# Optimization experiments

Hardware: AMD Instinct MI355X
Metric: run time of the kernel (lower is better)

The kernel has to match this reference:

```python
import jax, jax.numpy as jnp
import numpy as np

HEADS = 8
D_MODEL = 512

def setup_inputs() -> dict:
    key = jax.random.key(0)
    ks = jax.random.split(key, 7)
    t, w, h, b = 8, 14, 14, 8
    seq = t * w * h + 1  # 1569, includes CLS token
    q = jax.random.normal(ks[0], (seq, b, D_MODEL), jnp.float32)
    k = jax.random.normal(ks[1], (seq, b, D_MODEL), jnp.float32)
    value = jax.random.normal(ks[2], (seq, b, D_MODEL), jnp.float32)
    in_proj_weight = jax.random.normal(ks[3], (3 * D_MODEL, D_MODEL), jnp.float32) * (D_MODEL ** -0.5)
    in_proj_bias = jax.random.normal(ks[4], (3 * D_MODEL,), jnp.float32) * 0.02
    out_w = jax.random.normal(ks[5], (D_MODEL, D_MODEL), jnp.float32) * (D_MODEL ** -0.5)
    out_b = jax.random.normal(ks[6], (D_MODEL,), jnp.float32) * 0.02
    return {"q": q, "k": k, "value": value,
            "in_proj_weight": in_proj_weight, "in_proj_bias": in_proj_bias,
            "out_w": out_w, "out_b": out_b, "t": t, "w": w, "h": h}

def _sdpa(q, k, v):
    # scaled dot-product attention over batched 3D tensors [B, L, dh]
    temp = q.shape[-1] ** 0.5
    scores = jnp.einsum('bqd,bkd->bqk', q, k) / temp
    a = jax.nn.softmax(scores, axis=-1)  # softmax over dim=2 == last dim
    return jnp.einsum('bqk,bkd->bqd', a, v), a

def reference(q, k, value, in_proj_weight, in_proj_bias, out_w, out_b, t, w, h):
    seq, b, c = q.shape
    H, dh, wh = HEADS, c // HEADS, w * h
    q_cls = q[:1]          # [1, b, c] passed through untouched
    x = q[1:]              # [t*wh, b, c]
    qkv = x @ in_proj_weight.T + in_proj_bias  # fused QKV proj
    qq, kk, vv = qkv[..., :c], qkv[..., c:2 * c], qkv[..., 2 * c:]
    to5 = lambda z: z.reshape(t, wh, b, H, dh)
    # spatial stage: batch = (H, b, t), attend over wh
    q_s = to5(qq).transpose(3, 2, 0, 1, 4).reshape(H * b * t, wh, dh)
    k_s = to5(kk).transpose(3, 2, 0, 1, 4).reshape(H * b * t, wh, dh)
    v_s = to5(vv).transpose(3, 2, 0, 1, 4).reshape(H * b * t, wh, dh)
    out_s, attn = _sdpa(q_s, k_s, v_s)
    # temporal stage: batch = (H, b, wh), attend over t; V comes from spatial output
    v_t = out_s.reshape(H, b, t, wh, dh).transpose(0, 1, 3, 2, 4).reshape(H * b * wh, t, dh)
    q_t = to5(qq).transpose(3, 2, 1, 0, 4).reshape(H * b * wh, t, dh)
    k_t = to5(kk).transpose(3, 2, 1, 0, 4).reshape(H * b * wh, t, dh)
    out_t, _ = _sdpa(q_t, k_t, v_t)
    # back to [t*wh, b, c]
    out = out_t.reshape(H, b, wh, t, dh).transpose(3, 2, 1, 0, 4).reshape(t * wh, b, c)
    out = out @ out_w.T + out_b
    return jnp.concatenate([q_cls, out], axis=0), attn
```

## Files before the change

kernel.cpp:

```cpp
#include <hip/hip_runtime.h>
#include <cstdint>
#include <cstddef>

typedef __bf16 bf16;
typedef __bf16 bf16x8 __attribute__((ext_vector_type(8)));
typedef __bf16 bf16x4 __attribute__((ext_vector_type(4)));
typedef float  f32x4  __attribute__((ext_vector_type(4)));

#define MFMA16(a, b, c) __builtin_amdgcn_mfma_f32_16x16x32_bf16(a, b, c, 0, 0, 0)

__device__ __forceinline__ void gl2lds16(const bf16* g, bf16* l) {
  __builtin_amdgcn_global_load_lds(
      (const __attribute__((address_space(1))) void*)g,
      (__attribute__((address_space(3))) void*)l, 16, 0, 0);
}

__device__ __forceinline__ void cvt4(const float* __restrict__ s, bf16* __restrict__ d) {
  f32x4 v = *(const f32x4*)s;
  bf16x4 o;
  o[0] = (bf16)v[0]; o[1] = (bf16)v[1]; o[2] = (bf16)v[2]; o[3] = (bf16)v[3];
  *(bf16x4*)d = o;
}

__global__ __launch_bounds__(256) void prep_kernel(
    const float* __restrict__ q, const float* __restrict__ win,
    const float* __restrict__ wout, float* __restrict__ out0,
    bf16* __restrict__ xb, bf16* __restrict__ wqb, bf16* __restrict__ wob) {
  long u = (long)blockIdx.x * 256 + threadIdx.x;
  const long NX4 = 1605632, NWQ4 = 196608, NWO4 = 65536, NQC4 = 1024;
  if (u < NX4) { cvt4(q + 4096 + u * 4, xb + u * 4); return; }
  u -= NX4;
  if (u < NWQ4) { cvt4(win + u * 4, wqb + u * 4); return; }
  u -= NWQ4;
  if (u < NWO4) { cvt4(wout + u * 4, wob + u * 4); return; }
  u -= NWO4;
  if (u < NQC4) { *(f32x4*)(out0 + u * 4) = *(const f32x4*)(q + u * 4); }
}

template <bool OUTF32>
__global__ __launch_bounds__(256) void gemm_bt(
    const bf16* __restrict__ A, const bf16* __restrict__ Bm,
    const float* __restrict__ bias, bf16* __restrict__ Cb,
    float* __restrict__ Cf, int N, int K, long coff) {
  __shared__ bf16 As[128 * 32];
  __shared__ bf16 Bs[128 * 32];
  const int tid = threadIdx.x;
  const int wid = tid >> 6, lane = tid & 63;
  const int lr = lane & 15, lg = lane >> 4;

  const int nwg = gridDim.x * gridDim.y;
  const int orig = blockIdx.y * gridDim.x + blockIdx.x;
  const int cpx = nwg >> 3;
  const int swz = (orig & 7) * cpx + (orig >> 3);
  const int m0 = (swz / gridDim.x) * 128;
  const int n0 = (swz % gridDim.x) * 128;

  const int wr = wid >> 1, wc = wid & 1;
  const int srow = lane >> 2;
  const int scol = (lane & 3) * 8;

  f32x4 acc[4][4] = {};

  for (int kt = 0; kt < K; kt += 32) {
    __syncthreads();
#pragma unroll
    for (int j = 0; j < 2; ++j) {
      int r0 = wid * 32 + j * 16;
      gl2lds16(A + (size_t)(m0 + r0 + srow) * K + kt + scol, As + r0 * 32);
      gl2lds16(Bm + (size_t)(n0 + r0 + srow) * K + kt + scol, Bs + r0 * 32);
    }
    __syncthreads();

    bf16x8 af[4], bfr[4];
#pragma unroll
    for (int m = 0; m < 4; ++m)
      af[m] = *(const bf16x8*)(As + (wr * 64 + m * 16 + lr) * 32 + lg * 8);
#pragma unroll
    for (int n = 0; n < 4; ++n)
      bfr[n] = *(const bf16x8*)(Bs + (wc * 64 + n * 16 + lr) * 32 + lg * 8);
#pragma unroll
    for (int m = 0; m < 4; ++m)
#pragma unroll
      for (int n = 0; n < 4; ++n)
        acc[m][n] = MFMA16(af[m], bfr[n], acc[m][n]);
  }

#pragma unroll
  for (int m = 0; m < 4; ++m) {
    int row = m0 + wr * 64 + m * 16 + lg * 4;
#pragma unroll
    for (int n = 0; n < 4; ++n) {
      int col = n0 + wc * 64 + n * 16 + lr;
      float bv = bias[col];
#pragma unroll
      for (int i = 0; i < 4; ++i) {
        float v = acc[m][n][i] + bv;
        if (OUTF32)
          __builtin_nontemporal_store(v, Cf + coff + (size_t)(row + i) * N + col);
        else
          Cb[(size_t)(row + i) * N + col] = (bf16)v;
      }
    }
  }
}

__global__ __launch_bounds__(1024) void spatial_attn(
    const bf16* __restrict__ qkv, float* __restrict__ attn_out,
    bf16* __restrict__ outs) {
  __shared__ bf16 Kl[224 * 64];
  __shared__ bf16 Vt[64][232];
  __shared__ bf16 StgB[13 * 3136];

  const int tid = threadIdx.x;
  const int wid = tid >> 6, lane = tid & 63;
  const int lr = lane & 15, lg = lane >> 4;
  const int batch = blockIdx.x;
  const int ti = batch & 7;
  const int bb = (batch >> 3) & 7;
  const int h = batch >> 6;

  {
    const int slot = lane & 7, r8 = lane >> 3;
    const int chunk = slot ^ r8;
#pragma unroll
    for (int t = 0; t < 2; ++t) {
      int j = wid + t * 16;
      if (j < 28) {
        int row = j * 8 + r8;
        int grow = row > 195 ? 195 : row;
        const bf16* src = qkv +
            ((size_t)(ti * 196 + grow) * 8 + bb) * 1536 + h * 64 + 512 +
            chunk * 8;
        gl2lds16(src, Kl + j * 512);
      }
    }
  }
  {
    const int c = (wid & 7) * 8;
    const int rbase = (wid >> 3) * 64 + lane;
#pragma unroll
    for (int r0 = 0; r0 < 256; r0 += 128) {
      int pp = r0 + rbase;
      if (pp < 224) {
        int gp = pp > 195 ? 195 : pp;
        bf16x8 vv = *(const bf16x8*)(
            qkv + ((size_t)(ti * 196 + gp) * 8 + bb) * 1536 + h * 64 + 1024 + c);
#pragma unroll
        for (int j = 0; j < 8; ++j) Vt[c + j][pp] = vv[j];
      }
    }
  }

  const int qt = wid;
  bf16x8 aq[2];
  if (qt < 13) {
    int row = qt * 16 + lr;
    if (row > 195) row = 195;
    size_t ro = ((size_t)(ti * 196 + row) * 8 + bb) * 1536 + h * 64;
#pragma unroll
    for (int kk = 0; kk < 2; ++kk)
      aq[kk] = *(const bf16x8*)(qkv + ro + kk * 32 + lg * 8);
  }
  __syncthreads();

  if (qt < 13) {
    const int q = qt * 16 + lr;
    const int x7 = lr & 7;

    f32x4 s[14] = {};
    __builtin_amdgcn_s_setprio(1);
#pragma unroll
    for (int nn = 0; nn < 14; ++nn) {
      const int krow = nn * 16 + lr;
      bf16x8 bk0 = *(const bf16x8*)&Kl[krow * 64 + ((lg ^ x7) * 8)];
      bf16x8 bk1 = *(const bf16x8*)&Kl[krow * 64 + (((4 + lg) ^ x7) * 8)];
      s[nn] = MFMA16(bk0, aq[0], s[nn]);
      s[nn] = MFMA16(bk1, aq[1], s[nn]);
    }
    __builtin_amdgcn_s_setprio(0);

#pragma unroll
    for (int nn = 0; nn < 14; ++nn) {
      bool pad = (nn * 16 + lg * 4 >= 196);
#pragma unroll
      for (int i = 0; i < 4; ++i)
        s[nn][i] = pad ? -1e30f : s[nn][i] * 0.125f;
    }

    float v = -1e30f;
#pragma unroll
    for (int nn = 0; nn < 14; ++nn)
#pragma unroll
      for (int i = 0; i < 4; ++i) v = fmaxf(v, s[nn][i]);
    v = fmaxf(v, __shfl_xor(v, 16));
    v = fmaxf(v, __shfl_xor(v, 32));
    float sum = 0.f;
#pragma unroll
    for (int nn = 0; nn < 14; ++nn)
#pragma unroll
      for (int i = 0; i < 4; ++i) {
        float e = __expf(s[nn][i] - v);
        s[nn][i] = e;
        sum += e;
      }
    sum += __shfl_xor(sum, 16);
    sum += __shfl_xor(sum, 32);
    const float rinv = 1.f / sum;

    bf16* const tile = StgB + qt * 3136;
    const int low = lr + 32 * (lg & 1);
    const int high = low + 16;
    const bool hiN = (lg >> 1) != 0;
    f32x4 o[4] = {};
#pragma unroll
    for (int kb = 0; kb < 7; ++kb) {
      uint32_t px[2], py[2];
#pragma unroll
      for (int t = 0; t < 2; ++t) {
        const int nn = 2 * kb + t;
        f32x4 sv;
#pragma unroll
        for (int i = 0; i < 4; ++i) sv[i] = s[nn][i] * rinv;
        union { bf16x4 h; uint2 u; } pk;
        pk.h[0] = (bf16)sv[0]; pk.h[1] = (bf16)sv[1];
        pk.h[2] = (bf16)sv[2]; pk.h[3] = (bf16)sv[3];
        int kbase = nn * 16 + lg * 4;
        if (kbase < 196)
          *(uint2*)((char*)tile + lr * 392 + kbase * 2) = pk.u;
        px[t] = pk.u.x; py[t] = pk.u.y;
      }
      uint32_t a0x = __shfl((int)px[0], low);
      uint32_t a0y = __shfl((int)py[0], low);
      uint32_t a1x = __shfl((int)px[1], low);
      uint32_t a1y = __shfl((int)py[1], low);
      uint32_t b0x = __shfl((int)px[0], high);
      uint32_t b0y = __shfl((int)py[0], high);
      uint32_t b1x = __shfl((int)px[1], high);
      uint32_t b1y = __shfl((int)py[1], high);
      union { uint32_t u[4]; bf16x8 h; } pa;
      pa.u[0] = hiN ? a1x : a0x;
      pa.u[1] = hiN ? a1y : a0y;
      pa.u[2] = hiN ? b1x : b0x;
      pa.u[3] = hiN ? b1y : b0y;
      __builtin_amdgcn_s_setprio(1);
#pragma unroll
      for (int nd = 0; nd < 4; ++nd) {
        bf16x8 vb = *(const bf16x8*)&Vt[nd * 16 + lr][kb * 32 + lg * 8];
        o[nd] = MFMA16(pa.h, vb, o[nd]);
      }
      __builtin_amdgcn_s_setprio(0);
    }

#pragma unroll
    for (int i = 0; i < 4; ++i) {
      int p = qt * 16 + lg * 4 + i;
      if (p < 196) {
#pragma unroll
        for (int nd = 0; nd < 4; ++nd) {
          int d = nd * 16 + lr;
          outs[(((size_t)((h * 8 + bb) * 196 + p)) * 8 + ti) * 64 + d] =
              (bf16)o[nd][i];
        }
      }
    }

    {
      const int vbytes = (qt == 12) ? 3136 : 12544;
      char* dst = (char*)(attn_out + (size_t)batch * 38416 + qt * 3136);
      const char* src = (const char*)tile;
#pragma unroll
      for (int j = 0; j < 13; ++j) {
        int x = j * 1024 + lane * 16;
        if (x < vbytes) {
          uint2 u = *(const uint2*)(src + (x >> 1));
          union { uint32_t b; float f; } c0, c1, c2, c3;
          c0.b = (u.x & 0xffffu) << 16; c1.b = u.x & 0xffff0000u;
          c2.b = (u.y & 0xffffu) << 16; c3.b = u.y & 0xffff0000u;
          f32x4 ov; ov[0] = c0.f; ov[1] = c1.f; ov[2] = c2.f; ov[3] = c3.f;
          *(f32x4*)(dst + x) = ov;
        }
      }
    }
  }
}

__global__ __launch_bounds__(256) void temporal_attn(
    const bf16* __restrict__ qkv, const bf16* __restrict__ outs,
    bf16* __restrict__ outt) {
  __shared__ bf16 Ql[4][8][72];
  __shared__ bf16 Kc[4][8][72];
  __shared__ bf16 Vl[4][8][64];
  __shared__ float Ps[4][8][8];

  const int tid = threadIdx.x, wid = tid >> 6, lane = tid & 63;
  const int batch = blockIdx.x * 4 + wid;
  const int p = batch % 196;
  const int hb = batch / 196;
  const int bb = hb & 7, h = hb >> 3;

  const int ri = lane >> 3;
  const int c8 = lane & 7;
  {
    size_t ro = ((size_t)(ri * 196 + p) * 8 + bb) * 1536 + h * 64 + c8 * 8;
    *(bf16x8*)&Ql[wid][ri][c8 * 8] = *(const bf16x8*)(qkv + ro);
    *(bf16x8*)&Kc[wid][ri][c8 * 8] = *(const bf16x8*)(qkv + ro + 512);
    *(bf16x8*)&Vl[wid][ri][c8 * 8] =
        *(const bf16x8*)(outs + ((size_t)batch * 8 + ri) * 64 + c8 * 8);
  }
  __syncthreads();

  float s = 0.f;
#pragma unroll
  for (int d = 0; d < 64; d += 8) {
    bf16x8 qv = *(const bf16x8*)&Ql[wid][ri][d];
    bf16x8 kv = *(const bf16x8*)&Kc[wid][c8][d];
#pragma unroll
    for (int e = 0; e < 8; ++e) s += (float)qv[e] * (float)kv[e];
  }
  s *= 0.125f;
  float mxv = s;
#pragma unroll
  for (int d2 = 1; d2 < 8; d2 <<= 1) mxv = fmaxf(mxv, __shfl_xor(mxv, d2));
  float e = __expf(s - mxv);
  float sum = e;
#pragma unroll
  for (int d2 = 1; d2 < 8; d2 <<= 1) sum += __shfl_xor(sum, d2);
  Ps[wid][ri][c8] = e / sum;
  __syncthreads();

  const int d = lane;
#pragma unroll
  for (int ii = 0; ii < 8; ++ii) {
    float o = 0.f;
#pragma unroll
    for (int j = 0; j < 8; ++j) o += Ps[wid][ii][j] * (float)Vl[wid][j][d];
    outt[((size_t)(ii * 196 + p) * 8 + bb) * 512 + h * 64 + d] = (bf16)o;
  }
}

extern "C" void kernel_launch(void* const* d_in, const int* in_sizes, int n_in,
                              void* d_out, int out_size, void* d_ws,
                              size_t ws_size, hipStream_t stream) {
  (void)in_sizes; (void)n_in; (void)out_size; (void)ws_size;
  const float* q    = (const float*)d_in[0];
  const float* win  = (const float*)d_in[3];
  const float* bin  = (const float*)d_in[4];
  const float* wout = (const float*)d_in[5];
  const float* bout = (const float*)d_in[6];
  float* out0 = (float*)d_out;
  float* attn = out0 + 6426624L;

  bf16* qkv  = (bf16*)d_ws;
  bf16* outs = qkv + 19267584L;
  bf16* outt = outs + 6422528L;
  bf16* wob  = outt + 6422528L;

  bf16* xb  = (bf16*)attn;
  bf16* wqb = xb + 6422528L;

  prep_kernel<<<7300, 256, 0, stream>>>(q, win, wout, out0, xb, wqb, wob);
  gemm_bt<false><<<dim3(12, 98), 256, 0, stream>>>(xb, wqb, bin, qkv, nullptr,
                                                   1536, 512, 0);
  spatial_attn<<<512, 1024, 0, stream>>>(qkv, attn, outs);
  temporal_attn<<<3136, 256, 0, stream>>>(qkv, outs, outt);
  gemm_bt<true><<<dim3(4, 98), 256, 0, stream>>>(outt, wob, bout, nullptr,
                                                 out0, 512, 512, 4096);
}
```

Before: 102.4 us.

## Scatter QKV projection output into head-major per-batch slabs

The QKV GEMM epilogue now writes Q, K and V into separate head-major buffers laid out as [h,b,t][p][64], replacing the interleaved [seq,b,1536] output. The spatial attention kernel then reads each batch's Q/K/V as one contiguous 196x64 slab instead of strided 128-byte rows. The aim is more coalesced, contiguous reads in the attention kernels. In exchange the GEMM's stores become scattered 2-byte writes with integer division in the epilogue, and the temporal kernel's Q/K reads become strided across slabs.

```diff
diff --git a/kernel.cpp b/kernel.cpp
--- a/kernel.cpp
+++ b/kernel.cpp
@@ -40,7 +40,8 @@
 template <bool OUTF32>
 __global__ __launch_bounds__(256) void gemm_bt(
     const bf16* __restrict__ A, const bf16* __restrict__ Bm,
-    const float* __restrict__ bias, bf16* __restrict__ Cb,
+    const float* __restrict__ bias, bf16* __restrict__ Qh,
+    bf16* __restrict__ Kh, bf16* __restrict__ Vh,
     float* __restrict__ Cf, int N, int K, long coff) {
   __shared__ bf16 As[128 * 32];
   __shared__ bf16 Bs[128 * 32];
@@ -87,25 +88,36 @@
 
 #pragma unroll
   for (int m = 0; m < 4; ++m) {
-    int row = m0 + wr * 64 + m * 16 + lg * 4;
+    int rowb = m0 + wr * 64 + m * 16 + lg * 4;
 #pragma unroll
     for (int n = 0; n < 4; ++n) {
       int col = n0 + wc * 64 + n * 16 + lr;
       float bv = bias[col];
-#pragma unroll
-      for (int i = 0; i < 4; ++i) {
-        float v = acc[m][n][i] + bv;
-        if (OUTF32)
-          __builtin_nontemporal_store(v, Cf + coff + (size_t)(row + i) * N + col);
-        else
-          Cb[(size_t)(row + i) * N + col] = (bf16)v;
+      if (OUTF32) {
+#pragma unroll
+        for (int i = 0; i < 4; ++i)
+          __builtin_nontemporal_store(
+              acc[m][n][i] + bv, Cf + coff + (size_t)(rowb + i) * N + col);
+      } else {
+        int sec = col >> 9, c = col & 511;
+        int hh = c >> 6, dd = c & 63;
+        bf16* base = sec == 0 ? Qh : (sec == 1 ? Kh : Vh);
+#pragma unroll
+        for (int i = 0; i < 4; ++i) {
+          int r = rowb + i;
+          int ti2 = r / 1568, rem = r - ti2 * 1568;
+          int p2 = rem >> 3, b2 = rem & 7;
+          base[(size_t)(hh * 64 + b2 * 8 + ti2) * 12544 + p2 * 64 + dd] =
+              (bf16)(acc[m][n][i] + bv);
+        }
       }
     }
   }
 }
 
 __global__ __launch_bounds__(1024) void spatial_attn(
-    const bf16* __restrict__ qkv, float* __restrict__ attn_out,
+    const bf16* __restrict__ Qh, const bf16* __restrict__ Kh,
+    const bf16* __restrict__ Vh, float* __restrict__ attn_out,
     bf16* __restrict__ outs) {
   __shared__ bf16 Kl[224 * 64];
   __shared__ bf16 Vt[64][232];
@@ -115,9 +127,12 @@
   const int wid = tid >> 6, lane = tid & 63;
   const int lr = lane & 15, lg = lane >> 4;
   const int batch = blockIdx.x;
-  const int ti = batch & 7;
+  const bf16* slabQ = Qh + (size_t)batch * 12544;
+  const bf16* slabK = Kh + (size_t)batch * 12544;
+  const bf16* slabV = Vh + (size_t)batch * 12544;
+  const int h = batch >> 6;
   const int bb = (batch >> 3) & 7;
-  const int h = batch >> 6;
+  (void)h; (void)bb;
 
   {
     const int slot = lane & 7, r8 = lane >> 3;
@@ -128,10 +143,7 @@
       if (j < 28) {
         int row = j * 8 + r8;
         int grow = row > 195 ? 195 : row;
-        const bf16* src = qkv +
-            ((size_t)(ti * 196 + grow) * 8 + bb) * 1536 + h * 64 + 512 +
-            chunk * 8;
-        gl2lds16(src, Kl + j * 512);
+        gl2lds16(slabK + grow * 64 + chunk * 8, Kl + j * 512);
       }
     }
   }
@@ -143,8 +155,7 @@
       int pp = r0 + rbase;
       if (pp < 224) {
         int gp = pp > 195 ? 195 : pp;
-        bf16x8 vv = *(const bf16x8*)(
-            qkv + ((size_t)(ti * 196 + gp) * 8 + bb) * 1536 + h * 64 + 1024 + c);
+        bf16x8 vv = *(const bf16x8*)(slabV + gp * 64 + c);
 #pragma unroll
         for (int j = 0; j < 8; ++j) Vt[c + j][pp] = vv[j];
       }
@@ -156,10 +167,9 @@
   if (qt < 13) {
     int row = qt * 16 + lr;
     if (row > 195) row = 195;
-    size_t ro = ((size_t)(ti * 196 + row) * 8 + bb) * 1536 + h * 64;
 #pragma unroll
     for (int kk = 0; kk < 2; ++kk)
-      aq[kk] = *(const bf16x8*)(qkv + ro + kk * 32 + lg * 8);
+      aq[kk] = *(const bf16x8*)(slabQ + row * 64 + kk * 32 + lg * 8);
   }
   __syncthreads();
 
@@ -251,15 +261,19 @@
       __builtin_amdgcn_s_setprio(0);
     }
 
-#pragma unroll
-    for (int i = 0; i < 4; ++i) {
-      int p = qt * 16 + lg * 4 + i;
-      if (p < 196) {
-#pragma unroll
-        for (int nd = 0; nd < 4; ++nd) {
-          int d = nd * 16 + lr;
-          outs[(((size_t)((h * 8 + bb) * 196 + p)) * 8 + ti) * 64 + d] =
-              (bf16)o[nd][i];
+    {
+      const int hb8 = batch >> 3;
+      const int ti = batch & 7;
+#pragma unroll
+      for (int i = 0; i < 4; ++i) {
+        int p = qt * 16 + lg * 4 + i;
+        if (p < 196) {
+#pragma unroll
+          for (int nd = 0; nd < 4; ++nd) {
+            int d = nd * 16 + lr;
+            outs[(((size_t)(hb8 * 196 + p)) * 8 + ti) * 64 + d] =
+                (bf16)o[nd][i];
+          }
         }
       }
     }
@@ -285,8 +299,8 @@
 }
 
 __global__ __launch_bounds__(256) void temporal_attn(
-    const bf16* __restrict__ qkv, const bf16* __restrict__ outs,
-    bf16* __restrict__ outt) {
+    const bf16* __restrict__ Qh, const bf16* __restrict__ Kh,
+    const bf16* __restrict__ outs, bf16* __restrict__ outt) {
   __shared__ bf16 Ql[4][8][72];
   __shared__ bf16 Kc[4][8][72];
   __shared__ bf16 Vl[4][8][64];
@@ -301,9 +315,9 @@
   const int ri = lane >> 3;
   const int c8 = lane & 7;
   {
-    size_t ro = ((size_t)(ri * 196 + p) * 8 + bb) * 1536 + h * 64 + c8 * 8;
-    *(bf16x8*)&Ql[wid][ri][c8 * 8] = *(const bf16x8*)(qkv + ro);
-    *(bf16x8*)&Kc[wid][ri][c8 * 8] = *(const bf16x8*)(qkv + ro + 512);
+    size_t so = ((size_t)(h * 64 + bb * 8 + ri)) * 12544 + p * 64 + c8 * 8;
+    *(bf16x8*)&Ql[wid][ri][c8 * 8] = *(const bf16x8*)(Qh + so);
+    *(bf16x8*)&Kc[wid][ri][c8 * 8] = *(const bf16x8*)(Kh + so);
     *(bf16x8*)&Vl[wid][ri][c8 * 8] =
         *(const bf16x8*)(outs + ((size_t)batch * 8 + ri) * 64 + c8 * 8);
   }
@@ -350,8 +364,10 @@
   float* out0 = (float*)d_out;
   float* attn = out0 + 6426624L;
 
-  bf16* qkv  = (bf16*)d_ws;
-  bf16* outs = qkv + 19267584L;
+  bf16* Qh   = (bf16*)d_ws;
+  bf16* Kh   = Qh + 6422528L;
+  bf16* Vh   = Kh + 6422528L;
+  bf16* outs = Vh + 6422528L;
   bf16* outt = outs + 6422528L;
   bf16* wob  = outt + 6422528L;
 
@@ -359,10 +375,10 @@
   bf16* wqb = xb + 6422528L;
 
   prep_kernel<<<7300, 256, 0, stream>>>(q, win, wout, out0, xb, wqb, wob);
-  gemm_bt<false><<<dim3(12, 98), 256, 0, stream>>>(xb, wqb, bin, qkv, nullptr,
-                                                   1536, 512, 0);
-  spatial_attn<<<512, 1024, 0, stream>>>(qkv, attn, outs);
-  temporal_attn<<<3136, 256, 0, stream>>>(qkv, outs, outt);
-  gemm_bt<true><<<dim3(4, 98), 256, 0, stream>>>(outt, wob, bout, nullptr,
-                                                 out0, 512, 512, 4096);
-}
+  gemm_bt<false><<<dim3(12, 98), 256, 0, stream>>>(
+      xb, wqb, bin, Qh, Kh, Vh, nullptr, 1536, 512, 0);
+  spatial_attn<<<512, 1024, 0, stream>>>(Qh, Kh, Vh, attn, outs);
+  temporal_attn<<<3136, 256, 0, stream>>>(Qh, Kh, outs, outt);
+  gemm_bt<true><<<dim3(4, 98), 256, 0, stream>>>(
+      outt, wob, bout, nullptr, nullptr, nullptr, out0, 512, 512, 4096);
+}
```

Measured after the change: 103.3 us. No clear change (+0.9%).
